# Kernel optimization log

Measured on AMD Instinct MI355X. Metric: run time of the kernel, lower is better.

Reference implementation:

```python
import jax, jax.numpy as jnp
import numpy as np

H_IMG, W_IMG = 2160, 3840


def _avgpool3x3(x):
    # AvgPool2d(3, stride=1, padding=1), count_include_pad=True -> divide by 9 always
    s = jax.lax.reduce_window(x, 0.0, jax.lax.add, (3, 3, 1), (1, 1, 1), 'SAME')
    return s / 9.0


def setup_inputs() -> dict:
    key = jax.random.key(0)
    k1, k2, k3, k4 = jax.random.split(key, 4)
    depth = jax.random.uniform(k1, (H_IMG, W_IMG), jnp.float32) * 4.0 + 0.5
    rgb = jax.random.uniform(k2, (H_IMG, W_IMG, 3), jnp.float32)
    mask = jax.random.randint(k3, (H_IMG, W_IMG), 0, 2, jnp.int32)
    l = jax.random.normal(k4, (9, 3), jnp.float32) * 0.3
    fx = fy = 3000.0
    cx, cy = W_IMG / 2.0, H_IMG / 2.0
    CameraParam = jnp.array([[fx, 0.0, cx], [0.0, fy, cy], [0.0, 0.0, 1.0]], jnp.float32)
    return {'depth': depth, 'rgb': rgb, 'mask': mask, 'l': l, 'CameraParam': CameraParam}


def reference(depth, rgb, mask, l, CameraParam):
    nrows, ncols = depth.shape
    imask = mask > 0                      # [H, W] bool
    m3 = imask[..., None]                 # [H, W, 1]

    # Homogeneous pixel grid -> back-projected rays (precomputed in torch __init__)
    yy, xx = jnp.meshgrid(jnp.arange(nrows, dtype=jnp.float32),
                          jnp.arange(ncols, dtype=jnp.float32), indexing='ij')
    p2d = jnp.stack([xx, yy, jnp.ones_like(xx)], axis=-1)      # [H, W, 3]
    Kinv = jnp.linalg.inv(CameraParam)
    p3d = jnp.einsum('ij,hwj->hwi', Kinv, p2d)                 # [H, W, 3]

    # Depth -> 3D points, shifted neighbors (zero-padded at borders)
    p = p3d * depth[..., None]                                 # [H, W, 3]
    pl = jnp.pad(p[:, 1:, :], ((0, 0), (0, 1), (0, 0)))        # right neighbor
    pu = jnp.pad(p[1:, :, :], ((0, 1), (0, 0), (0, 0)))        # down neighbor

    n = jnp.cross(pl - p, pu - p)                              # [H, W, 3]
    norm = jnp.linalg.norm(n, axis=-1, keepdims=True)
    n = n / jnp.maximum(norm, 1e-12)                           # F.normalize

    nx, ny, nz = n[..., 0], n[..., 1], n[..., 2]
    ones = jnp.ones_like(nx)
    Hsh = jnp.stack([ones, ny, nz, nx, nx * ny, ny * nz,
                     -nx * nx - ny * ny + 2.0 * nz * nz,
                     nz * nx, nx * nx - ny * ny], axis=-1)     # [H, W, 9]
    B = jnp.einsum('hwk,kc->hwc', Hsh, l)                      # [H, W, 3]

    # Scatter into full image: zero outside mask (matches render_img[imask] = B)
    render = jnp.where(m3, B, 0.0)
    render_mean = jax.lax.stop_gradient(_avgpool3x3(render))   # render_img.detach()
    rgbmean = _avgpool3x3(jax.lax.stop_gradient(rgb))          # rgb.detach()

    diff = (render - render_mean) - (rgb - rgbmean)
    cnt = jnp.sum(imask).astype(jnp.float32) * 3.0             # MSE over masked elems
    loss = jnp.sum(jnp.where(m3, diff * diff, 0.0)) / cnt
    return loss
```

## Files before the change

### kernel.cpp

```cpp
#include <hip/hip_runtime.h>
#include <math.h>

#define H_IMG 2160
#define W_IMG 3840
#define TW 32
#define TH 8
#define EW (TW + 2)
#define EH (TH + 2)
#define NBINS 2048

__global__ __launch_bounds__(256) void shading_main(
    const float* __restrict__ depth,
    const float* __restrict__ rgb,
    const int*   __restrict__ mask,
    const float* __restrict__ lmat,
    const float* __restrict__ K,
    float* __restrict__ accum)
{
    __shared__ float q[EH][EW][3];
    __shared__ float sS[4], sC[4];

    const int tx  = threadIdx.x;
    const int ty  = threadIdx.y;
    const int tid = ty * TW + tx;
    const int w0  = blockIdx.x * TW;
    const int h0  = blockIdx.y * TH;

    const float m00 = K[0], m01 = K[1], m02 = K[2];
    const float m10 = K[3], m11 = K[4], m12 = K[5];
    const float m20 = K[6], m21 = K[7], m22 = K[8];
    const float det = m00*(m11*m22 - m12*m21)
                    - m01*(m10*m22 - m12*m20)
                    + m02*(m10*m21 - m11*m20);
    const float id  = 1.0f / det;
    const float i00 = (m11*m22 - m12*m21) * id;
    const float i01 = (m02*m21 - m01*m22) * id;
    const float i02 = (m01*m12 - m02*m11) * id;
    const float i10 = (m12*m20 - m10*m22) * id;
    const float i11 = (m00*m22 - m02*m20) * id;
    const float i12 = (m02*m10 - m00*m12) * id;
    const float i20 = (m10*m21 - m11*m20) * id;
    const float i21 = (m01*m20 - m00*m21) * id;
    const float i22 = (m00*m11 - m01*m10) * id;

    float L[27];
    #pragma unroll
    for (int i = 0; i < 27; ++i) L[i] = lmat[i];

    for (int idx = tid; idx < EH * EW; idx += TW * TH) {
        const int er = idx / EW;
        const int ec = idx - er * EW;
        const int gh = h0 - 1 + er;
        const int gw = w0 - 1 + ec;
        float q0 = 0.f, q1 = 0.f, q2 = 0.f;
        if (gh >= 0 && gh < H_IMG && gw >= 0 && gw < W_IMG) {
            const int pix = gh * W_IMG + gw;
            const float r0 = rgb[pix*3+0], r1 = rgb[pix*3+1], r2 = rgb[pix*3+2];
            const int   mv = mask[pix];

            const float fw = (float)gw, fh = (float)gh;
            const float dxr = i00*fw + i01*fh + i02;
            const float dyr = i10*fw + i11*fh + i12;
            const float dzr = i20*fw + i21*fh + i22;

            const float d0 = depth[pix];
            const float px = dxr*d0, py = dyr*d0, pz = dzr*d0;

            float plx = 0.f, ply = 0.f, plz = 0.f;
            if (gw + 1 < W_IMG) {
                const float dl = depth[pix + 1];
                plx = (dxr + i00) * dl;
                ply = (dyr + i10) * dl;
                plz = (dzr + i20) * dl;
            }
            float pux = 0.f, puy = 0.f, puz = 0.f;
            if (gh + 1 < H_IMG) {
                const float du = depth[pix + W_IMG];
                pux = (dxr + i01) * du;
                puy = (dyr + i11) * du;
                puz = (dzr + i21) * du;
            }

            const float ax = plx - px, ay = ply - py, az = plz - pz;
            const float bx = pux - px, by = puy - py, bz = puz - pz;
            float nx = ay*bz - az*by;
            float ny = az*bx - ax*bz;
            float nz = ax*by - ay*bx;
            const float nn  = nx*nx + ny*ny + nz*nz;
            const float inr = 1.0f / fmaxf(sqrtf(nn), 1e-12f);
            nx *= inr; ny *= inr; nz *= inr;

            const float h4 = nx*ny, h5 = ny*nz, h7 = nz*nx;
            const float h6 = -nx*nx - ny*ny + 2.0f*nz*nz;
            const float h8 =  nx*nx - ny*ny;

            float B0 = L[0] + ny*L[3] + nz*L[6] + nx*L[9]  + h4*L[12] + h5*L[15] + h6*L[18] + h7*L[21] + h8*L[24];
            float B1 = L[1] + ny*L[4] + nz*L[7] + nx*L[10] + h4*L[13] + h5*L[16] + h6*L[19] + h7*L[22] + h8*L[25];
            float B2 = L[2] + ny*L[5] + nz*L[8] + nx*L[11] + h4*L[14] + h5*L[17] + h6*L[20] + h7*L[23] + h8*L[26];
            if (mv <= 0) { B0 = 0.f; B1 = 0.f; B2 = 0.f; }

            q0 = B0 - r0; q1 = B1 - r1; q2 = B2 - r2;
        }
        q[er][ec][0] = q0;
        q[er][ec][1] = q1;
        q[er][ec][2] = q2;
    }
    __syncthreads();

    const int gh  = h0 + ty;
    const int gw  = w0 + tx;
    const int pix = gh * W_IMG + gw;

    float s0 = 0.f, s1 = 0.f, s2 = 0.f;
    #pragma unroll
    for (int dy2 = 0; dy2 < 3; ++dy2) {
        #pragma unroll
        for (int dx2 = 0; dx2 < 3; ++dx2) {
            s0 += q[ty + dy2][tx + dx2][0];
            s1 += q[ty + dy2][tx + dx2][1];
            s2 += q[ty + dy2][tx + dx2][2];
        }
    }
    const float c0 = q[ty+1][tx+1][0] - s0 * (1.0f/9.0f);
    const float c1 = q[ty+1][tx+1][1] - s1 * (1.0f/9.0f);
    const float c2 = q[ty+1][tx+1][2] - s2 * (1.0f/9.0f);

    float S = 0.f, C = 0.f;
    if (mask[pix] > 0) {
        S = c0*c0 + c1*c1 + c2*c2;
        C = 1.f;
    }

    #pragma unroll
    for (int off = 32; off > 0; off >>= 1) {
        S += __shfl_down(S, off, 64);
        C += __shfl_down(C, off, 64);
    }
    const int wid = tid >> 6, lane = tid & 63;
    if (lane == 0) { sS[wid] = S; sC[wid] = C; }
    __syncthreads();
    if (tid == 0) {
        const float ts = sS[0] + sS[1] + sS[2] + sS[3];
        const float tc = sC[0] + sC[1] + sC[2] + sC[3];
        const int bin = (blockIdx.y * gridDim.x + blockIdx.x) & (NBINS - 1);
        atomicAdd(&accum[2*bin + 0], ts);
        atomicAdd(&accum[2*bin + 1], tc);
    }
}

__global__ __launch_bounds__(256) void finalize_kernel(
    const float* __restrict__ accum, float* __restrict__ out)
{
    const int tid = threadIdx.x;
    float s = 0.f, c = 0.f;
    for (int i = tid; i < NBINS; i += 256) {
        s += accum[2*i + 0];
        c += accum[2*i + 1];
    }
    #pragma unroll
    for (int off = 32; off > 0; off >>= 1) {
        s += __shfl_down(s, off, 64);
        c += __shfl_down(c, off, 64);
    }
    __shared__ float sS[4], sC[4];
    const int wid = tid >> 6, lane = tid & 63;
    if (lane == 0) { sS[wid] = s; sC[wid] = c; }
    __syncthreads();
    if (tid == 0) {
        const float ts = sS[0] + sS[1] + sS[2] + sS[3];
        const float tc = sC[0] + sC[1] + sC[2] + sC[3];
        out[0] = ts / (3.0f * tc);
    }
}

extern "C" void kernel_launch(void* const* d_in, const int* in_sizes, int n_in,
                              void* d_out, int out_size, void* d_ws, size_t ws_size,
                              hipStream_t stream) {
    const float* depth = (const float*)d_in[0];
    const float* rgb   = (const float*)d_in[1];
    const int*   mask  = (const int*)  d_in[2];
    const float* lmat  = (const float*)d_in[3];
    const float* K     = (const float*)d_in[4];
    float* accum = (float*)d_ws;
    float* out   = (float*)d_out;

    hipMemsetAsync(accum, 0, NBINS * 2 * sizeof(float), stream);

    dim3 block(TW, TH);
    dim3 grid(W_IMG / TW, H_IMG / TH);
    shading_main<<<grid, block, 0, stream>>>(depth, rgb, mask, lmat, K, accum);
    finalize_kernel<<<1, 256, 0, stream>>>(accum, out);
}
```

Baseline: 233.9 us.

## Enlarge tiles, vectorize halo loads, column-reuse 3x3 sums, write per-block partials

Tiles grow to 64x16 pixels per 256-thread block. Each thread now shades four pixels using float4 loads of depth, mask and rgb, and the shaded residual and mask are stored as float4 in padded shared memory. The 3x3 box sum is computed by each thread over a 4-row column strip, reusing row sums, which cuts the halo recompute overhead. Normalization uses the rsq intrinsic instead of sqrt plus divide. When the workspace is large enough, per-block partials are written directly, which drops the memset and the atomics, and finalize reduces about 8100 partials. Risks include more shared memory per block lowering occupancy, and slight precision differences from rsq.

```diff
diff --git a/kernel.cpp b/kernel.cpp
--- a/kernel.cpp
+++ b/kernel.cpp
@@ -3,11 +3,48 @@
 
 #define H_IMG 2160
 #define W_IMG 3840
-#define TW 32
-#define TH 8
-#define EW (TW + 2)
-#define EH (TH + 2)
+#define TW 64
+#define TH 16
+#define EXT_ROWS 18
+#define EXT_COLS 72
+#define QPITCH 73
+#define NGROUPS 18
+#define NUNITS (EXT_ROWS * NGROUPS)
 #define NBINS 2048
+
+__device__ __forceinline__ float4 shade_px(
+    float rx, float ry, float rz,
+    float i00, float i10, float i20,
+    float i01, float i11, float i21,
+    float d0, float dR, float dD,
+    float maskf, float r0, float r1, float r2,
+    const float (&L)[27])
+{
+    const float px = rx * d0, py = ry * d0, pz = rz * d0;
+    const float ax = (rx + i00) * dR - px;
+    const float ay = (ry + i10) * dR - py;
+    const float az = (rz + i20) * dR - pz;
+    const float bx = (rx + i01) * dD - px;
+    const float by = (ry + i11) * dD - py;
+    const float bz = (rz + i21) * dD - pz;
+    float nx = ay * bz - az * by;
+    float ny = az * bx - ax * bz;
+    float nz = ax * by - ay * bx;
+    const float nn  = nx * nx + ny * ny + nz * nz;
+    const float inr = __builtin_amdgcn_rsqf(fmaxf(nn, 1e-24f));
+    nx *= inr; ny *= inr; nz *= inr;
+    const float h4 = nx * ny, h5 = ny * nz, h7 = nz * nx;
+    const float nx2 = nx * nx, ny2 = ny * ny, nz2 = nz * nz;
+    const float h6 = 2.0f * nz2 - nx2 - ny2;
+    const float h8 = nx2 - ny2;
+    const float B0 = L[0] + ny*L[3] + nz*L[6] + nx*L[9]  + h4*L[12] + h5*L[15] + h6*L[18] + h7*L[21] + h8*L[24];
+    const float B1 = L[1] + ny*L[4] + nz*L[7] + nx*L[10] + h4*L[13] + h5*L[16] + h6*L[19] + h7*L[22] + h8*L[25];
+    const float B2 = L[2] + ny*L[5] + nz*L[8] + nx*L[11] + h4*L[14] + h5*L[17] + h6*L[20] + h7*L[23] + h8*L[26];
+    return make_float4(fmaf(maskf, B0, -r0),
+                       fmaf(maskf, B1, -r1),
+                       fmaf(maskf, B2, -r2),
+                       maskf);
+}
 
 __global__ __launch_bounds__(256) void shading_main(
     const float* __restrict__ depth,
@@ -15,14 +52,13 @@
     const int*   __restrict__ mask,
     const float* __restrict__ lmat,
     const float* __restrict__ K,
-    float* __restrict__ accum)
+    float* __restrict__ accum,
+    int direct)
 {
-    __shared__ float q[EH][EW][3];
+    __shared__ float4 qs[EXT_ROWS * QPITCH];
     __shared__ float sS[4], sC[4];
 
-    const int tx  = threadIdx.x;
-    const int ty  = threadIdx.y;
-    const int tid = ty * TW + tx;
+    const int tid = threadIdx.x;
     const int w0  = blockIdx.x * TW;
     const int h0  = blockIdx.y * TH;
 
@@ -47,88 +83,92 @@
     #pragma unroll
     for (int i = 0; i < 27; ++i) L[i] = lmat[i];
 
-    for (int idx = tid; idx < EH * EW; idx += TW * TH) {
-        const int er = idx / EW;
-        const int ec = idx - er * EW;
-        const int gh = h0 - 1 + er;
-        const int gw = w0 - 1 + ec;
-        float q0 = 0.f, q1 = 0.f, q2 = 0.f;
-        if (gh >= 0 && gh < H_IMG && gw >= 0 && gw < W_IMG) {
-            const int pix = gh * W_IMG + gw;
-            const float r0 = rgb[pix*3+0], r1 = rgb[pix*3+1], r2 = rgb[pix*3+2];
-            const int   mv = mask[pix];
-
-            const float fw = (float)gw, fh = (float)gh;
-            const float dxr = i00*fw + i01*fh + i02;
-            const float dyr = i10*fw + i11*fh + i12;
-            const float dzr = i20*fw + i21*fh + i22;
-
-            const float d0 = depth[pix];
-            const float px = dxr*d0, py = dyr*d0, pz = dzr*d0;
-
-            float plx = 0.f, ply = 0.f, plz = 0.f;
-            if (gw + 1 < W_IMG) {
-                const float dl = depth[pix + 1];
-                plx = (dxr + i00) * dl;
-                ply = (dyr + i10) * dl;
-                plz = (dzr + i20) * dl;
+    for (unsigned u = tid; u < NUNITS; u += 256) {
+        const unsigned r = u / 18u;
+        const unsigned j = u - r * 18u;
+        const int gh  = h0 - 1 + (int)r;
+        const int gw0 = w0 - 4 + (int)(j * 4u);
+        float4* dst = &qs[r * QPITCH + j * 4u];
+
+        const bool fast = (gh >= 0) & (gh < H_IMG) & (gw0 >= 0) & (gw0 + 4 < W_IMG);
+        if (fast) {
+            const int pix = gh * W_IMG + gw0;
+            const float4 dc = *(const float4*)(depth + pix);
+            const float dr4 = depth[pix + 4];
+            float4 dn = make_float4(0.f, 0.f, 0.f, 0.f);
+            if (gh + 1 < H_IMG) dn = *(const float4*)(depth + pix + W_IMG);
+            const int4  mv = *(const int4*)(mask + pix);
+            const float4 ra = *(const float4*)(rgb + pix * 3);
+            const float4 rb = *(const float4*)(rgb + pix * 3 + 4);
+            const float4 rc = *(const float4*)(rgb + pix * 3 + 8);
+
+            float rx = fmaf(i00, (float)gw0, fmaf(i01, (float)gh, i02));
+            float ry = fmaf(i10, (float)gw0, fmaf(i11, (float)gh, i12));
+            float rz = fmaf(i20, (float)gw0, fmaf(i21, (float)gh, i22));
+
+            const float dcur[5] = {dc.x, dc.y, dc.z, dc.w, dr4};
+            const float ddn[4]  = {dn.x, dn.y, dn.z, dn.w};
+            const float rr[12]  = {ra.x, ra.y, ra.z, ra.w,
+                                   rb.x, rb.y, rb.z, rb.w,
+                                   rc.x, rc.y, rc.z, rc.w};
+            const int   mm[4]   = {mv.x, mv.y, mv.z, mv.w};
+            #pragma unroll
+            for (int k = 0; k < 4; ++k) {
+                const float mf = (mm[k] > 0) ? 1.0f : 0.0f;
+                dst[k] = shade_px(rx, ry, rz, i00, i10, i20, i01, i11, i21,
+                                  dcur[k], dcur[k + 1], ddn[k],
+                                  mf, rr[3*k], rr[3*k+1], rr[3*k+2], L);
+                rx += i00; ry += i10; rz += i20;
             }
-            float pux = 0.f, puy = 0.f, puz = 0.f;
-            if (gh + 1 < H_IMG) {
-                const float du = depth[pix + W_IMG];
-                pux = (dxr + i01) * du;
-                puy = (dyr + i11) * du;
-                puz = (dzr + i21) * du;
+        } else {
+            #pragma unroll
+            for (int k = 0; k < 4; ++k) {
+                const int gw = gw0 + k;
+                float4 qv = make_float4(0.f, 0.f, 0.f, 0.f);
+                if (gh >= 0 && gh < H_IMG && gw >= 0 && gw < W_IMG) {
+                    const int pix = gh * W_IMG + gw;
+                    const float d0 = depth[pix];
+                    const float dR = (gw + 1 < W_IMG) ? depth[pix + 1] : 0.0f;
+                    const float dD = (gh + 1 < H_IMG) ? depth[pix + W_IMG] : 0.0f;
+                    const float mf = (mask[pix] > 0) ? 1.0f : 0.0f;
+                    const float r0 = rgb[pix*3], r1 = rgb[pix*3+1], r2 = rgb[pix*3+2];
+                    const float rx = fmaf(i00, (float)gw, fmaf(i01, (float)gh, i02));
+                    const float ry = fmaf(i10, (float)gw, fmaf(i11, (float)gh, i12));
+                    const float rz = fmaf(i20, (float)gw, fmaf(i21, (float)gh, i22));
+                    qv = shade_px(rx, ry, rz, i00, i10, i20, i01, i11, i21,
+                                  d0, dR, dD, mf, r0, r1, r2, L);
+                }
+                dst[k] = qv;
             }
-
-            const float ax = plx - px, ay = ply - py, az = plz - pz;
-            const float bx = pux - px, by = puy - py, bz = puz - pz;
-            float nx = ay*bz - az*by;
-            float ny = az*bx - ax*bz;
-            float nz = ax*by - ay*bx;
-            const float nn  = nx*nx + ny*ny + nz*nz;
-            const float inr = 1.0f / fmaxf(sqrtf(nn), 1e-12f);
-            nx *= inr; ny *= inr; nz *= inr;
-
-            const float h4 = nx*ny, h5 = ny*nz, h7 = nz*nx;
-            const float h6 = -nx*nx - ny*ny + 2.0f*nz*nz;
-            const float h8 =  nx*nx - ny*ny;
-
-            float B0 = L[0] + ny*L[3] + nz*L[6] + nx*L[9]  + h4*L[12] + h5*L[15] + h6*L[18] + h7*L[21] + h8*L[24];
-            float B1 = L[1] + ny*L[4] + nz*L[7] + nx*L[10] + h4*L[13] + h5*L[16] + h6*L[19] + h7*L[22] + h8*L[25];
-            float B2 = L[2] + ny*L[5] + nz*L[8] + nx*L[11] + h4*L[14] + h5*L[17] + h6*L[20] + h7*L[23] + h8*L[26];
-            if (mv <= 0) { B0 = 0.f; B1 = 0.f; B2 = 0.f; }
-
-            q0 = B0 - r0; q1 = B1 - r1; q2 = B2 - r2;
         }
-        q[er][ec][0] = q0;
-        q[er][ec][1] = q1;
-        q[er][ec][2] = q2;
     }
     __syncthreads();
 
-    const int gh  = h0 + ty;
-    const int gw  = w0 + tx;
-    const int pix = gh * W_IMG + gw;
-
-    float s0 = 0.f, s1 = 0.f, s2 = 0.f;
-    #pragma unroll
-    for (int dy2 = 0; dy2 < 3; ++dy2) {
-        #pragma unroll
-        for (int dx2 = 0; dx2 < 3; ++dx2) {
-            s0 += q[ty + dy2][tx + dx2][0];
-            s1 += q[ty + dy2][tx + dx2][1];
-            s2 += q[ty + dy2][tx + dx2][2];
-        }
-    }
-    const float c0 = q[ty+1][tx+1][0] - s0 * (1.0f/9.0f);
-    const float c1 = q[ty+1][tx+1][1] - s1 * (1.0f/9.0f);
-    const float c2 = q[ty+1][tx+1][2] - s2 * (1.0f/9.0f);
-
+    const int tx = tid & 63;
+    const int tq = tid >> 6;
+    float rs0[6], rs1[6], rs2[6];
+    float4 cv[4];
+    #pragma unroll
+    for (int r = 0; r < 6; ++r) {
+        const float4* rowp = &qs[(4 * tq + r) * QPITCH + tx + 3];
+        const float4 a = rowp[0], b = rowp[1], c = rowp[2];
+        rs0[r] = a.x + b.x + c.x;
+        rs1[r] = a.y + b.y + c.y;
+        rs2[r] = a.z + b.z + c.z;
+        if (r >= 1 && r <= 4) cv[r - 1] = b;
+    }
     float S = 0.f, C = 0.f;
-    if (mask[pix] > 0) {
-        S = c0*c0 + c1*c1 + c2*c2;
-        C = 1.f;
+    #pragma unroll
+    for (int k = 0; k < 4; ++k) {
+        const float s0 = rs0[k] + rs0[k+1] + rs0[k+2];
+        const float s1 = rs1[k] + rs1[k+1] + rs1[k+2];
+        const float s2 = rs2[k] + rs2[k+1] + rs2[k+2];
+        const float d0 = cv[k].x - s0 * (1.0f/9.0f);
+        const float d1 = cv[k].y - s1 * (1.0f/9.0f);
+        const float d2 = cv[k].z - s2 * (1.0f/9.0f);
+        const float m  = cv[k].w;
+        S = fmaf(m, d0*d0 + d1*d1 + d2*d2, S);
+        C += m;
     }
 
     #pragma unroll
@@ -142,20 +182,26 @@
     if (tid == 0) {
         const float ts = sS[0] + sS[1] + sS[2] + sS[3];
         const float tc = sC[0] + sC[1] + sC[2] + sC[3];
-        const int bin = (blockIdx.y * gridDim.x + blockIdx.x) & (NBINS - 1);
-        atomicAdd(&accum[2*bin + 0], ts);
-        atomicAdd(&accum[2*bin + 1], tc);
+        const int bid = blockIdx.y * gridDim.x + blockIdx.x;
+        if (direct) {
+            accum[2*bid + 0] = ts;
+            accum[2*bid + 1] = tc;
+        } else {
+            const int bin = bid & (NBINS - 1);
+            atomicAdd(&accum[2*bin + 0], ts);
+            atomicAdd(&accum[2*bin + 1], tc);
+        }
     }
 }
 
 __global__ __launch_bounds__(256) void finalize_kernel(
-    const float* __restrict__ accum, float* __restrict__ out)
+    const float* __restrict__ part, int n, float* __restrict__ out)
 {
     const int tid = threadIdx.x;
     float s = 0.f, c = 0.f;
-    for (int i = tid; i < NBINS; i += 256) {
-        s += accum[2*i + 0];
-        c += accum[2*i + 1];
+    for (int i = tid; i < n; i += 256) {
+        s += part[2*i + 0];
+        c += part[2*i + 1];
     }
     #pragma unroll
     for (int off = 32; off > 0; off >>= 1) {
@@ -184,10 +230,15 @@
     float* accum = (float*)d_ws;
     float* out   = (float*)d_out;
 
-    hipMemsetAsync(accum, 0, NBINS * 2 * sizeof(float), stream);
-
-    dim3 block(TW, TH);
-    dim3 grid(W_IMG / TW, H_IMG / TH);
-    shading_main<<<grid, block, 0, stream>>>(depth, rgb, mask, lmat, K, accum);
-    finalize_kernel<<<1, 256, 0, stream>>>(accum, out);
-}
+    const dim3 grid(W_IMG / TW, H_IMG / TH);
+    const int nblocks = (W_IMG / TW) * (H_IMG / TH);
+
+    if (ws_size >= (size_t)nblocks * 2 * sizeof(float)) {
+        shading_main<<<grid, 256, 0, stream>>>(depth, rgb, mask, lmat, K, accum, 1);
+        finalize_kernel<<<1, 256, 0, stream>>>(accum, nblocks, out);
+    } else {
+        hipMemsetAsync(accum, 0, NBINS * 2 * sizeof(float), stream);
+        shading_main<<<grid, 256, 0, stream>>>(depth, rgb, mask, lmat, K, accum, 0);
+        finalize_kernel<<<1, 256, 0, stream>>>(accum, NBINS, out);
+    }
+}
```

After: 211.7 us. 1.1x faster.

## Restructure into register-resident vertical strips with shuffle-based 3x3 stencil

Applied to the files above, without the earlier changes.

Replaces the shared-memory 2D tile (which recomputed the halo ring per block) with wavefronts that each own a 256-column strip of 10 rows. Each lane handles 4 consecutive pixels loaded with float4 vectors and slides down the rows, keeping the last three rows of partial sums in registers. Horizontal neighbours are exchanged with lane shuffles, so halo recompute and LDS traffic are removed. It also uses a hardware rsq, writes per-block partials directly instead of memset plus atomics when workspace allows, and sets an occupancy launch bound, at the cost of high register pressure from full unrolling.

```diff
diff --git a/kernel.cpp b/kernel.cpp
--- a/kernel.cpp
+++ b/kernel.cpp
@@ -3,28 +3,31 @@
 
 #define H_IMG 2160
 #define W_IMG 3840
-#define TW 32
-#define TH 8
-#define EW (TW + 2)
-#define EH (TH + 2)
+#define SPAN 252
+#define NSX 16
+#define HS 10
+#define WPB 4
+#define NSY 54
+#define NBLOCKS (NSX * NSY)
 #define NBINS 2048
 
-__global__ __launch_bounds__(256) void shading_main(
+__global__ __launch_bounds__(256, 3) void shading_main(
     const float* __restrict__ depth,
     const float* __restrict__ rgb,
     const int*   __restrict__ mask,
     const float* __restrict__ lmat,
     const float* __restrict__ K,
-    float* __restrict__ accum)
+    float* __restrict__ accum,
+    int direct)
 {
-    __shared__ float q[EH][EW][3];
-    __shared__ float sS[4], sC[4];
-
-    const int tx  = threadIdx.x;
-    const int ty  = threadIdx.y;
-    const int tid = ty * TW + tx;
-    const int w0  = blockIdx.x * TW;
-    const int h0  = blockIdx.y * TH;
+    const int tid  = threadIdx.x;
+    const int lane = tid & 63;
+    const int wv   = tid >> 6;
+    const int sx   = blockIdx.x;
+    const int x0   = sx * SPAN;
+    const int y0   = (blockIdx.y * WPB + wv) * HS;
+    const int colBase = x0 + 4 * lane;
+    const bool fullIn = (colBase + 3) < W_IMG;
 
     const float m00 = K[0], m01 = K[1], m02 = K[2];
     const float m10 = K[3], m11 = K[4], m12 = K[5];
@@ -47,115 +50,180 @@
     #pragma unroll
     for (int i = 0; i < 27; ++i) L[i] = lmat[i];
 
-    for (int idx = tid; idx < EH * EW; idx += TW * TH) {
-        const int er = idx / EW;
-        const int ec = idx - er * EW;
-        const int gh = h0 - 1 + er;
-        const int gw = w0 - 1 + ec;
-        float q0 = 0.f, q1 = 0.f, q2 = 0.f;
-        if (gh >= 0 && gh < H_IMG && gw >= 0 && gw < W_IMG) {
-            const int pix = gh * W_IMG + gw;
-            const float r0 = rgb[pix*3+0], r1 = rgb[pix*3+1], r2 = rgb[pix*3+2];
-            const int   mv = mask[pix];
-
-            const float fw = (float)gw, fh = (float)gh;
-            const float dxr = i00*fw + i01*fh + i02;
-            const float dyr = i10*fw + i11*fh + i12;
-            const float dzr = i20*fw + i21*fh + i22;
-
-            const float d0 = depth[pix];
-            const float px = dxr*d0, py = dyr*d0, pz = dzr*d0;
-
-            float plx = 0.f, ply = 0.f, plz = 0.f;
-            if (gw + 1 < W_IMG) {
-                const float dl = depth[pix + 1];
-                plx = (dxr + i00) * dl;
-                ply = (dyr + i10) * dl;
-                plz = (dzr + i20) * dl;
+    float wout[4];
+    #pragma unroll
+    for (int k = 0; k < 4; ++k) {
+        const int c  = colBase + k;
+        const int lc = 4 * lane + k;
+        const bool v = (c < W_IMG) && (lc <= SPAN) && (lc >= 1 || sx == 0);
+        wout[k] = v ? 1.0f : 0.0f;
+    }
+    const float qm1s = (lane == 0) ? 0.0f : 1.0f;
+
+    float rx = fmaf(i00, (float)colBase, fmaf(i01, (float)(y0 - 1), i02));
+    float ry = fmaf(i10, (float)colBase, fmaf(i11, (float)(y0 - 1), i12));
+    float rz = fmaf(i20, (float)colBase, fmaf(i21, (float)(y0 - 1), i22));
+
+    float dc[4] = {0.f, 0.f, 0.f, 0.f};
+    if (fullIn && y0 > 0) {
+        const float4 t = *(const float4*)(depth + (long)(y0 - 1) * W_IMG + colBase);
+        dc[0] = t.x; dc[1] = t.y; dc[2] = t.z; dc[3] = t.w;
+    }
+
+    float s0s[3][4], s1s[3][4], s2s[3][4];
+    float qc0[3][4], qc1[3][4], qc2[3][4], qcw[3][4];
+    float accS = 0.f, accC = 0.f;
+
+    #pragma unroll
+    for (int j = 0; j < HS + 2; ++j) {
+        const int h  = y0 - 1 + j;
+        const int hn = h + 1;
+        const int sl = j % 3;
+
+        float dn[4] = {0.f, 0.f, 0.f, 0.f};
+        float rr[12] = {0.f, 0.f, 0.f, 0.f, 0.f, 0.f, 0.f, 0.f, 0.f, 0.f, 0.f, 0.f};
+        float mf[4] = {0.f, 0.f, 0.f, 0.f};
+        if (fullIn) {
+            if (hn < H_IMG) {
+                const float4 t = *(const float4*)(depth + (long)hn * W_IMG + colBase);
+                dn[0] = t.x; dn[1] = t.y; dn[2] = t.z; dn[3] = t.w;
             }
-            float pux = 0.f, puy = 0.f, puz = 0.f;
-            if (gh + 1 < H_IMG) {
-                const float du = depth[pix + W_IMG];
-                pux = (dxr + i01) * du;
-                puy = (dyr + i11) * du;
-                puz = (dzr + i21) * du;
+            if ((unsigned)h < (unsigned)H_IMG) {
+                const long pix = (long)h * W_IMG + colBase;
+                const float4 a  = *(const float4*)(rgb + pix * 3);
+                const float4 b  = *(const float4*)(rgb + pix * 3 + 4);
+                const float4 cc = *(const float4*)(rgb + pix * 3 + 8);
+                const int4   mm = *(const int4*)(mask + pix);
+                rr[0] = a.x;  rr[1] = a.y;  rr[2]  = a.z;
+                rr[3] = a.w;  rr[4] = b.x;  rr[5]  = b.y;
+                rr[6] = b.z;  rr[7] = b.w;  rr[8]  = cc.x;
+                rr[9] = cc.y; rr[10] = cc.z; rr[11] = cc.w;
+                mf[0] = mm.x > 0 ? 1.f : 0.f;
+                mf[1] = mm.y > 0 ? 1.f : 0.f;
+                mf[2] = mm.z > 0 ? 1.f : 0.f;
+                mf[3] = mm.w > 0 ? 1.f : 0.f;
             }
-
-            const float ax = plx - px, ay = ply - py, az = plz - pz;
-            const float bx = pux - px, by = puy - py, bz = puz - pz;
+        }
+        const float dcR = __shfl_down(dc[0], 1, 64);
+
+        float rxk = rx, ryk = ry, rzk = rz;
+        #pragma unroll
+        for (int k = 0; k < 4; ++k) {
+            const float d0 = dc[k];
+            const float dR = (k < 3) ? dc[k + 1] : dcR;
+            const float dD = dn[k];
+            const float px = rxk * d0, py = ryk * d0, pz = rzk * d0;
+            const float ax = (rxk + i00) * dR - px;
+            const float ay = (ryk + i10) * dR - py;
+            const float az = (rzk + i20) * dR - pz;
+            const float bx = (rxk + i01) * dD - px;
+            const float by = (ryk + i11) * dD - py;
+            const float bz = (rzk + i21) * dD - pz;
             float nx = ay*bz - az*by;
             float ny = az*bx - ax*bz;
             float nz = ax*by - ay*bx;
             const float nn  = nx*nx + ny*ny + nz*nz;
-            const float inr = 1.0f / fmaxf(sqrtf(nn), 1e-12f);
+            const float inr = __builtin_amdgcn_rsqf(fmaxf(nn, 1e-24f));
             nx *= inr; ny *= inr; nz *= inr;
-
             const float h4 = nx*ny, h5 = ny*nz, h7 = nz*nx;
-            const float h6 = -nx*nx - ny*ny + 2.0f*nz*nz;
-            const float h8 =  nx*nx - ny*ny;
-
-            float B0 = L[0] + ny*L[3] + nz*L[6] + nx*L[9]  + h4*L[12] + h5*L[15] + h6*L[18] + h7*L[21] + h8*L[24];
-            float B1 = L[1] + ny*L[4] + nz*L[7] + nx*L[10] + h4*L[13] + h5*L[16] + h6*L[19] + h7*L[22] + h8*L[25];
-            float B2 = L[2] + ny*L[5] + nz*L[8] + nx*L[11] + h4*L[14] + h5*L[17] + h6*L[20] + h7*L[23] + h8*L[26];
-            if (mv <= 0) { B0 = 0.f; B1 = 0.f; B2 = 0.f; }
-
-            q0 = B0 - r0; q1 = B1 - r1; q2 = B2 - r2;
-        }
-        q[er][ec][0] = q0;
-        q[er][ec][1] = q1;
-        q[er][ec][2] = q2;
-    }
-    __syncthreads();
-
-    const int gh  = h0 + ty;
-    const int gw  = w0 + tx;
-    const int pix = gh * W_IMG + gw;
-
-    float s0 = 0.f, s1 = 0.f, s2 = 0.f;
-    #pragma unroll
-    for (int dy2 = 0; dy2 < 3; ++dy2) {
-        #pragma unroll
-        for (int dx2 = 0; dx2 < 3; ++dx2) {
-            s0 += q[ty + dy2][tx + dx2][0];
-            s1 += q[ty + dy2][tx + dx2][1];
-            s2 += q[ty + dy2][tx + dx2][2];
-        }
-    }
-    const float c0 = q[ty+1][tx+1][0] - s0 * (1.0f/9.0f);
-    const float c1 = q[ty+1][tx+1][1] - s1 * (1.0f/9.0f);
-    const float c2 = q[ty+1][tx+1][2] - s2 * (1.0f/9.0f);
-
-    float S = 0.f, C = 0.f;
-    if (mask[pix] > 0) {
-        S = c0*c0 + c1*c1 + c2*c2;
-        C = 1.f;
+            const float nx2 = nx*nx, ny2 = ny*ny, nz2 = nz*nz;
+            const float h6 = 2.f*nz2 - nx2 - ny2;
+            const float h8 = nx2 - ny2;
+            const float B0 = L[0] + ny*L[3] + nz*L[6] + nx*L[9]  + h4*L[12] + h5*L[15] + h6*L[18] + h7*L[21] + h8*L[24];
+            const float B1 = L[1] + ny*L[4] + nz*L[7] + nx*L[10] + h4*L[13] + h5*L[16] + h6*L[19] + h7*L[22] + h8*L[25];
+            const float B2 = L[2] + ny*L[5] + nz*L[8] + nx*L[11] + h4*L[14] + h5*L[17] + h6*L[20] + h7*L[23] + h8*L[26];
+            const float m  = mf[k];
+            qc0[sl][k] = fmaf(m, B0, -rr[3*k + 0]);
+            qc1[sl][k] = fmaf(m, B1, -rr[3*k + 1]);
+            qc2[sl][k] = fmaf(m, B2, -rr[3*k + 2]);
+            qcw[sl][k] = m * wout[k];
+            rxk += i00; ryk += i10; rzk += i20;
+        }
+
+        {
+            const float a0 = __shfl_up(qc0[sl][3], 1, 64) * qm1s;
+            const float a1 = __shfl_up(qc1[sl][3], 1, 64) * qm1s;
+            const float a2 = __shfl_up(qc2[sl][3], 1, 64) * qm1s;
+            const float p0 = __shfl_down(qc0[sl][0], 1, 64);
+            const float p1 = __shfl_down(qc1[sl][0], 1, 64);
+            const float p2 = __shfl_down(qc2[sl][0], 1, 64);
+
+            const float t01_0 = qc0[sl][0] + qc0[sl][1];
+            const float t12_0 = qc0[sl][1] + qc0[sl][2];
+            const float t23_0 = qc0[sl][2] + qc0[sl][3];
+            s0s[sl][0] = a0 + t01_0;
+            s0s[sl][1] = t01_0 + qc0[sl][2];
+            s0s[sl][2] = t12_0 + qc0[sl][3];
+            s0s[sl][3] = t23_0 + p0;
+
+            const float t01_1 = qc1[sl][0] + qc1[sl][1];
+            const float t12_1 = qc1[sl][1] + qc1[sl][2];
+            const float t23_1 = qc1[sl][2] + qc1[sl][3];
+            s1s[sl][0] = a1 + t01_1;
+            s1s[sl][1] = t01_1 + qc1[sl][2];
+            s1s[sl][2] = t12_1 + qc1[sl][3];
+            s1s[sl][3] = t23_1 + p1;
+
+            const float t01_2 = qc2[sl][0] + qc2[sl][1];
+            const float t12_2 = qc2[sl][1] + qc2[sl][2];
+            const float t23_2 = qc2[sl][2] + qc2[sl][3];
+            s2s[sl][0] = a2 + t01_2;
+            s2s[sl][1] = t01_2 + qc2[sl][2];
+            s2s[sl][2] = t12_2 + qc2[sl][3];
+            s2s[sl][3] = t23_2 + p2;
+        }
+
+        if (j >= 2) {
+            const int sA = (j - 2) % 3, sB = (j - 1) % 3;
+            #pragma unroll
+            for (int k = 0; k < 4; ++k) {
+                const float v0 = s0s[sA][k] + s0s[sB][k] + s0s[sl][k];
+                const float v1 = s1s[sA][k] + s1s[sB][k] + s1s[sl][k];
+                const float v2 = s2s[sA][k] + s2s[sB][k] + s2s[sl][k];
+                const float d0 = fmaf(v0, -(1.f/9.f), qc0[sB][k]);
+                const float d1 = fmaf(v1, -(1.f/9.f), qc1[sB][k]);
+                const float d2 = fmaf(v2, -(1.f/9.f), qc2[sB][k]);
+                const float w  = qcw[sB][k];
+                accS = fmaf(w, d0*d0 + d1*d1 + d2*d2, accS);
+                accC += w;
+            }
+        }
+
+        dc[0] = dn[0]; dc[1] = dn[1]; dc[2] = dn[2]; dc[3] = dn[3];
+        rx += i01; ry += i11; rz += i21;
     }
 
     #pragma unroll
     for (int off = 32; off > 0; off >>= 1) {
-        S += __shfl_down(S, off, 64);
-        C += __shfl_down(C, off, 64);
-    }
-    const int wid = tid >> 6, lane = tid & 63;
-    if (lane == 0) { sS[wid] = S; sC[wid] = C; }
+        accS += __shfl_down(accS, off, 64);
+        accC += __shfl_down(accC, off, 64);
+    }
+    __shared__ float sS[WPB], sC[WPB];
+    if (lane == 0) { sS[wv] = accS; sC[wv] = accC; }
     __syncthreads();
     if (tid == 0) {
         const float ts = sS[0] + sS[1] + sS[2] + sS[3];
         const float tc = sC[0] + sC[1] + sC[2] + sC[3];
-        const int bin = (blockIdx.y * gridDim.x + blockIdx.x) & (NBINS - 1);
-        atomicAdd(&accum[2*bin + 0], ts);
-        atomicAdd(&accum[2*bin + 1], tc);
+        const int bid = blockIdx.y * gridDim.x + blockIdx.x;
+        if (direct) {
+            accum[2*bid + 0] = ts;
+            accum[2*bid + 1] = tc;
+        } else {
+            const int bin = bid & (NBINS - 1);
+            atomicAdd(&accum[2*bin + 0], ts);
+            atomicAdd(&accum[2*bin + 1], tc);
+        }
     }
 }
 
 __global__ __launch_bounds__(256) void finalize_kernel(
-    const float* __restrict__ accum, float* __restrict__ out)
+    const float* __restrict__ part, int n, float* __restrict__ out)
 {
     const int tid = threadIdx.x;
     float s = 0.f, c = 0.f;
-    for (int i = tid; i < NBINS; i += 256) {
-        s += accum[2*i + 0];
-        c += accum[2*i + 1];
+    for (int i = tid; i < n; i += 256) {
+        s += part[2*i + 0];
+        c += part[2*i + 1];
     }
     #pragma unroll
     for (int off = 32; off > 0; off >>= 1) {
@@ -184,10 +252,14 @@
     float* accum = (float*)d_ws;
     float* out   = (float*)d_out;
 
-    hipMemsetAsync(accum, 0, NBINS * 2 * sizeof(float), stream);
-
-    dim3 block(TW, TH);
-    dim3 grid(W_IMG / TW, H_IMG / TH);
-    shading_main<<<grid, block, 0, stream>>>(depth, rgb, mask, lmat, K, accum);
-    finalize_kernel<<<1, 256, 0, stream>>>(accum, out);
+    const dim3 grid(NSX, NSY);
+
+    if (ws_size >= (size_t)NBLOCKS * 2 * sizeof(float)) {
+        shading_main<<<grid, 256, 0, stream>>>(depth, rgb, mask, lmat, K, accum, 1);
+        finalize_kernel<<<1, 256, 0, stream>>>(accum, NBLOCKS, out);
+    } else {
+        hipMemsetAsync(accum, 0, NBINS * 2 * sizeof(float), stream);
+        shading_main<<<grid, 256, 0, stream>>>(depth, rgb, mask, lmat, K, accum, 0);
+        finalize_kernel<<<1, 256, 0, stream>>>(accum, NBINS, out);
+    }
 }
```

Measured after the change: 360.0 us. +53.9%, slower.
